# Optimization experiments

Measured on AMD Instinct MI355X. Metric: run time of the kernel, lower is better.

## Reference

```python
import jax, jax.numpy as jnp
import numpy as np

N, E, F, H, G = 50000, 640000, 128, 128, 64


def setup_inputs() -> dict:
    key = jax.random.key(0)
    ks = jax.random.split(key, 10)
    x = jax.random.normal(ks[0], (N, F), dtype=jnp.float32)
    edge_index = jax.random.randint(ks[1], (2, E), 0, N)
    batch = jnp.sort(jax.random.randint(ks[2], (N,), 0, G))

    def glorot(k, shp):
        return jax.random.normal(k, shp, dtype=jnp.float32) * np.float32(1.0 / np.sqrt(shp[0]))

    W1 = glorot(ks[3], (F, H)); b1 = jnp.zeros((H,), jnp.float32)
    W2 = glorot(ks[4], (H, H)); b2 = jnp.zeros((H,), jnp.float32)
    W3 = glorot(ks[5], (H, H)); b3 = jnp.zeros((H,), jnp.float32)
    W4 = glorot(ks[6], (H, 2)); b4 = jnp.zeros((2,), jnp.float32)
    return {"x": x, "W1": W1, "b1": b1, "W2": W2, "b2": b2,
            "W3": W3, "b3": b3, "W4": W4, "b4": b4,
            "edge_index": edge_index, "batch": batch, "num_graphs": G}


def reference(x, W1, b1, W2, b2, W3, b3, W4, b4, edge_index, batch, num_graphs):
    n = x.shape[0]
    loop = jnp.arange(n, dtype=edge_index.dtype)
    src = jnp.concatenate([edge_index[0], loop])  # with self-loops (PyG GCNConv default)
    dst = jnp.concatenate([edge_index[1], loop])
    # symmetric degree normalization: D^{-1/2} (A+I) D^{-1/2}
    deg = jax.ops.segment_sum(jnp.ones_like(src, dtype=x.dtype), dst, num_segments=n)
    dinv = jnp.where(deg > 0, jax.lax.rsqrt(deg), 0.0)
    norm = (dinv[src] * dinv[dst])[:, None]  # [E+N, 1]

    def gcn_conv(h, W, b):
        m = h @ W                                   # transform first (F->H), then propagate
        agg = jax.ops.segment_sum(m[src] * norm, dst, num_segments=n)
        return agg + b

    h = jax.nn.relu(gcn_conv(x, W1, b1))
    h = jax.nn.relu(gcn_conv(h, W2, b2))
    g = jax.ops.segment_max(h, batch, num_segments=num_graphs)  # global_max_pool
    z = jax.nn.relu(g @ W3 + b3)                    # dropout is identity in eval
    logits = z @ W4 + b4
    return jax.nn.log_softmax(logits, axis=1)
```

## Files before the change

### kernel.cpp

```cpp
#include <hip/hip_runtime.h>
#include <hip/hip_bf16.h>
#include <math.h>

#define HDIM 128
#define SCAN_B 256
#define NBLK 256

typedef short bfrag __attribute__((ext_vector_type(8)));
typedef float f32x4 __attribute__((ext_vector_type(4)));

__device__ inline unsigned short f2bf_rne(float x) {
    unsigned u = __float_as_uint(x);
    u = (u + 0x7fffu + ((u >> 16) & 1u)) >> 16;
    return (unsigned short)u;
}
__device__ inline float bf_lo(unsigned u) { return __uint_as_float(u << 16); }
__device__ inline float bf_hi(unsigned u) { return __uint_as_float(u & 0xffff0000u); }


__device__ inline void hist_body(int b, const int* __restrict__ dst,
                                 int* __restrict__ hist, int E, int chunk) {
    int start = b * chunk, end = min(E, start + chunk);
    for (int e = start + threadIdx.x; e < end; e += 256)
        atomicAdd(&hist[dst[e]], 1);
}

__device__ inline void wfrag_body(int b, const float* __restrict__ W1,
                                  const float* __restrict__ W2,
                                  unsigned short* __restrict__ w1h,
                                  unsigned short* __restrict__ w1l,
                                  unsigned short* __restrict__ w2h,
                                  unsigned short* __restrict__ w2l) {
    const float* W = (b < 64) ? W1 : W2;
    unsigned short* whi = (b < 64) ? w1h : w2h;
    unsigned short* wlo = (b < 64) ? w1l : w2l;
    int idx = (b & 63) * 256 + threadIdx.x;
    int k = idx >> 7;
    int n = idx & 127;
    int kt = k >> 5, q = (k >> 3) & 3, j = k & 7;
    int lm = n >> 3, nt = n & 7;
    int lane = q * 16 + lm;
    int o = ((kt * 8 + nt) * 64 + lane) * 8 + j;
    float x = W[idx];
    unsigned short hb = f2bf_rne(x);
    float hf = __uint_as_float(((unsigned)hb) << 16);
    unsigned short lb = f2bf_rne(x - hf);
    whi[o] = hb;
    wlo[o] = lb;
}

__device__ inline void scatter_body(int b, const int* __restrict__ srcv,
                                    const int* __restrict__ dstv,
                                    int* __restrict__ cursor,
                                    int* __restrict__ csr,
                                    int E, int chunk) {
    int start = b * chunk, end = min(E, start + chunk);
    for (int e = start + threadIdx.x; e < end; e += 256) {
        int pos = atomicAdd(&cursor[dstv[e]], 1);
        csr[pos] = srcv[e];
    }
}

#define GBM 64
__device__ inline void gemm_f32_body(int b, const float* __restrict__ A,
                                     const unsigned short* __restrict__ whi,
                                     const unsigned short* __restrict__ wlo,
                                     const float* __restrict__ dinv,
                                     unsigned short* __restrict__ C, int Nrows) {
    int tid = threadIdx.x;
    int w = tid >> 6, L = tid & 63;
    int lm = L & 15, lq = L >> 4;
    int row0 = b * GBM + w * 16;

    f32x4 acc[8];
#pragma unroll
    for (int nt = 0; nt < 8; ++nt) acc[nt] = (f32x4)(0.f);

#pragma unroll
    for (int kt = 0; kt < 4; ++kt) {
        int gr = row0 + lm;
        float4 v0 = make_float4(0.f, 0.f, 0.f, 0.f);
        float4 v1 = v0;
        if (gr < Nrows) {
            const float* p = &A[(size_t)gr * HDIM + kt * 32 + lq * 8];
            v0 = *(const float4*)p;
            v1 = *(const float4*)(p + 4);
        }
        float xv[8] = {v0.x, v0.y, v0.z, v0.w, v1.x, v1.y, v1.z, v1.w};
        bfrag ah, al;
#pragma unroll
        for (int j = 0; j < 8; ++j) {
            float x = xv[j];
            unsigned short hb = f2bf_rne(x);
            float hf = __uint_as_float(((unsigned)hb) << 16);
            unsigned short lb = f2bf_rne(x - hf);
            ah[j] = (short)hb;
            al[j] = (short)lb;
        }
#pragma unroll
        for (int nt = 0; nt < 8; ++nt) {
            int o = ((kt * 8 + nt) * 64 + L) * 8;
            bfrag wh = *(const bfrag*)&whi[o];
            bfrag wl = *(const bfrag*)&wlo[o];
            acc[nt] = __builtin_amdgcn_mfma_f32_16x16x32_bf16(ah, wh, acc[nt], 0, 0, 0);
            acc[nt] = __builtin_amdgcn_mfma_f32_16x16x32_bf16(al, wh, acc[nt], 0, 0, 0);
            acc[nt] = __builtin_amdgcn_mfma_f32_16x16x32_bf16(ah, wl, acc[nt], 0, 0, 0);
        }
    }

#pragma unroll
    for (int i = 0; i < 4; ++i) {
        int gr = row0 + lq * 4 + i;
        if (gr < Nrows) {
            float dd = dinv[gr];
            bfrag e;
#pragma unroll
            for (int nt = 0; nt < 8; ++nt) e[nt] = (short)f2bf_rne(dd * acc[nt][i]);
            *(bfrag*)&C[(size_t)gr * HDIM + lm * 8] = e;
        }
    }
}

__global__ __launch_bounds__(256) void mega1_kernel(const int* __restrict__ dst,
                                                    int* __restrict__ hist, int E,
                                                    int chunk,
                                                    const float* __restrict__ W1,
                                                    const float* __restrict__ W2,
                                                    unsigned short* __restrict__ w1h,
                                                    unsigned short* __restrict__ w1l,
                                                    unsigned short* __restrict__ w2h,
                                                    unsigned short* __restrict__ w2l) {
    int b = blockIdx.x;
    if (b < NBLK) hist_body(b, dst, hist, E, chunk);
    else wfrag_body(b - NBLK, W1, W2, w1h, w1l, w2h, w2l);
}

__global__ __launch_bounds__(256) void mega3_kernel(const int* __restrict__ srcv,
                                                    const int* __restrict__ dstv,
                                                    int* __restrict__ cursor,
                                                    int* __restrict__ csr,
                                                    int E, int chunk,
                                                    const float* __restrict__ A,
                                                    const unsigned short* __restrict__ whi,
                                                    const unsigned short* __restrict__ wlo,
                                                    const float* __restrict__ dinv,
                                                    unsigned short* __restrict__ C, int Nrows) {
    int b = blockIdx.x;
    if (b < NBLK) scatter_body(b, srcv, dstv, cursor, csr, E, chunk);
    else gemm_f32_body(b - NBLK, A, whi, wlo, dinv, C, Nrows);
}

__global__ __launch_bounds__(SCAN_B) void scan1_kernel(const int* __restrict__ in,
                                                       int* __restrict__ out,
                                                       int* __restrict__ sums, int n) {
    __shared__ int s[SCAN_B];
    int t = threadIdx.x;
    int idx = blockIdx.x * SCAN_B + t;
    int v = (idx < n) ? in[idx] : 0;
    s[t] = v;
    __syncthreads();
    for (int off = 1; off < SCAN_B; off <<= 1) {
        int x = (t >= off) ? s[t - off] : 0;
        __syncthreads();
        s[t] += x;
        __syncthreads();
    }
    if (idx < n) out[idx] = s[t];
    if (t == SCAN_B - 1) sums[blockIdx.x] = s[t];
}

__global__ __launch_bounds__(SCAN_B) void scan3_kernel(const int* __restrict__ in,
                                                       const int* __restrict__ incl,
                                                       const int* __restrict__ sums,
                                                       int* __restrict__ rowstart,
                                                       int* __restrict__ cursor,
                                                       float* __restrict__ dinv,
                                                       int n, int E) {
    __shared__ int s[SCAN_B];
    int t = threadIdx.x;
    int b = blockIdx.x;
    s[t] = (t < b) ? sums[t] : 0;
    __syncthreads();
    for (int off = SCAN_B / 2; off > 0; off >>= 1) {
        if (t < off) s[t] += s[t + off];
        __syncthreads();
    }
    int base = s[0];
    int idx = b * SCAN_B + t;
    if (idx < n) {
        int d = in[idx];
        int excl = incl[idx] - d + base;
        rowstart[idx] = excl;
        cursor[idx] = excl;
        dinv[idx] = rsqrtf((float)(d + 1));
        if (idx == n - 1) rowstart[idx + 1] = E;
    }
}

#define QACC(UV)                                       \
    acc[0] += bf_lo((UV).x); acc[1] += bf_hi((UV).x);  \
    acc[2] += bf_lo((UV).y); acc[3] += bf_hi((UV).y);  \
    acc[4] += bf_lo((UV).z); acc[5] += bf_hi((UV).z);  \
    acc[6] += bf_lo((UV).w); acc[7] += bf_hi((UV).w);

__device__ inline void qgather(const uint4* __restrict__ m4,
                               const int* __restrict__ csr,
                               int p, int pend, int t, float* acc) {
    for (; p + 8 <= pend; p += 8) {
        int s0 = csr[p], s1 = csr[p + 1], s2 = csr[p + 2], s3 = csr[p + 3];
        int s4 = csr[p + 4], s5 = csr[p + 5], s6 = csr[p + 6], s7 = csr[p + 7];
        uint4 u0 = m4[(size_t)s0 * 16 + t];
        uint4 u1 = m4[(size_t)s1 * 16 + t];
        uint4 u2 = m4[(size_t)s2 * 16 + t];
        uint4 u3 = m4[(size_t)s3 * 16 + t];
        uint4 u4 = m4[(size_t)s4 * 16 + t];
        uint4 u5 = m4[(size_t)s5 * 16 + t];
        uint4 u6 = m4[(size_t)s6 * 16 + t];
        uint4 u7 = m4[(size_t)s7 * 16 + t];
        QACC(u0); QACC(u1); QACC(u2); QACC(u3);
        QACC(u4); QACC(u5); QACC(u6); QACC(u7);
    }
    if (p + 4 <= pend) {
        int s0 = csr[p], s1 = csr[p + 1], s2 = csr[p + 2], s3 = csr[p + 3];
        uint4 u0 = m4[(size_t)s0 * 16 + t];
        uint4 u1 = m4[(size_t)s1 * 16 + t];
        uint4 u2 = m4[(size_t)s2 * 16 + t];
        uint4 u3 = m4[(size_t)s3 * 16 + t];
        QACC(u0); QACC(u1); QACC(u2); QACC(u3);
        p += 4;
    }
    if (p + 2 <= pend) {
        int s0 = csr[p], s1 = csr[p + 1];
        uint4 u0 = m4[(size_t)s0 * 16 + t];
        uint4 u1 = m4[(size_t)s1 * 16 + t];
        QACC(u0); QACC(u1);
        p += 2;
    }
    if (p < pend) {
        int s0 = csr[p];
        uint4 u0 = m4[(size_t)s0 * 16 + t];
        QACC(u0);
    }
}

__global__ __launch_bounds__(256) void agg_gemm_kernel(
        const uint4* __restrict__ m4,
        const int* __restrict__ rowstart,
        const int* __restrict__ csr,
        const float* __restrict__ dinv,
        const float* __restrict__ bias,
        const unsigned short* __restrict__ whi,
        const unsigned short* __restrict__ wlo,
        uint4* __restrict__ out_m, int n) {
    __shared__ unsigned short hbuf[16][HDIM + 8];
    __shared__ float cbuf[16][HDIM + 4];
    int t = threadIdx.x & 15;
    int nl = threadIdx.x >> 4;
    int node = blockIdx.x * 16 + nl;

    float dd = 0.f;
    unsigned short hv[8] = {0, 0, 0, 0, 0, 0, 0, 0};
    if (node < n) {
        dd = dinv[node];
        float acc[8];
        uint4 u = m4[(size_t)node * 16 + t];
        acc[0] = bf_lo(u.x); acc[1] = bf_hi(u.x);
        acc[2] = bf_lo(u.y); acc[3] = bf_hi(u.y);
        acc[4] = bf_lo(u.z); acc[5] = bf_hi(u.z);
        acc[6] = bf_lo(u.w); acc[7] = bf_hi(u.w);
        qgather(m4, csr, rowstart[node], rowstart[node + 1], t, acc);
        float4 b0 = *(const float4*)&bias[t * 8];
        float4 b1 = *(const float4*)&bias[t * 8 + 4];
        float bb[8] = {b0.x, b0.y, b0.z, b0.w, b1.x, b1.y, b1.z, b1.w};
#pragma unroll
        for (int j = 0; j < 8; ++j)
            hv[j] = f2bf_rne(fmaxf(fmaf(dd, acc[j], bb[j]), 0.f));
    }
    *(uint4*)&hbuf[nl][t * 8] = *(uint4*)hv;
    __syncthreads();

    int w = threadIdx.x >> 6, L = threadIdx.x & 63;
    int lm = L & 15, lq = L >> 4;
    f32x4 acc2[2];
    acc2[0] = (f32x4)(0.f);
    acc2[1] = (f32x4)(0.f);
#pragma unroll
    for (int kt = 0; kt < 4; ++kt) {
        bfrag a = *(const bfrag*)&hbuf[lm][kt * 32 + lq * 8];
#pragma unroll
        for (int q2 = 0; q2 < 2; ++q2) {
            int nt = w * 2 + q2;
            int o = ((kt * 8 + nt) * 64 + L) * 8;
            bfrag wh = *(const bfrag*)&whi[o];
            bfrag wl = *(const bfrag*)&wlo[o];
            acc2[q2] = __builtin_amdgcn_mfma_f32_16x16x32_bf16(a, wh, acc2[q2], 0, 0, 0);
            acc2[q2] = __builtin_amdgcn_mfma_f32_16x16x32_bf16(a, wl, acc2[q2], 0, 0, 0);
        }
    }
#pragma unroll
    for (int q2 = 0; q2 < 2; ++q2) {
        int nt = w * 2 + q2;
#pragma unroll
        for (int i = 0; i < 4; ++i) cbuf[lq * 4 + i][lm * 8 + nt] = acc2[q2][i];
    }
    __syncthreads();

    if (node < n) {
        float4 r0 = *(const float4*)&cbuf[nl][t * 8];
        float4 r1 = *(const float4*)&cbuf[nl][t * 8 + 4];
        unsigned short ev[8];
        ev[0] = f2bf_rne(dd * r0.x); ev[1] = f2bf_rne(dd * r0.y);
        ev[2] = f2bf_rne(dd * r0.z); ev[3] = f2bf_rne(dd * r0.w);
        ev[4] = f2bf_rne(dd * r1.x); ev[5] = f2bf_rne(dd * r1.y);
        ev[6] = f2bf_rne(dd * r1.z); ev[7] = f2bf_rne(dd * r1.w);
        out_m[(size_t)node * 16 + t] = *(uint4*)ev;
    }
}

__global__ __launch_bounds__(256) void agg_pool_kernel(const uint4* __restrict__ m4,
                                                       const int* __restrict__ rowstart,
                                                       const int* __restrict__ csr,
                                                       const float* __restrict__ dinv,
                                                       const float* __restrict__ bias,
                                                       const int* __restrict__ batch,
                                                       unsigned int* __restrict__ g, int n) {
    __shared__ float smx[16][HDIM];
    __shared__ int sgid[16];
    int t = threadIdx.x & 15;
    int nl = threadIdx.x >> 4;
    int node = blockIdx.x * 16 + nl;
    bool valid = node < n;
    if (valid) {
        float dd = dinv[node];
        float acc[8];
        uint4 u = m4[(size_t)node * 16 + t];
        acc[0] = bf_lo(u.x); acc[1] = bf_hi(u.x);
        acc[2] = bf_lo(u.y); acc[3] = bf_hi(u.y);
        acc[4] = bf_lo(u.z); acc[5] = bf_hi(u.z);
        acc[6] = bf_lo(u.w); acc[7] = bf_hi(u.w);
        qgather(m4, csr, rowstart[node], rowstart[node + 1], t, acc);
        float4 b0 = *(const float4*)&bias[t * 8];
        float4 b1 = *(const float4*)&bias[t * 8 + 4];
        float4 r0, r1;
        r0.x = fmaxf(fmaf(dd, acc[0], b0.x), 0.f);
        r0.y = fmaxf(fmaf(dd, acc[1], b0.y), 0.f);
        r0.z = fmaxf(fmaf(dd, acc[2], b0.z), 0.f);
        r0.w = fmaxf(fmaf(dd, acc[3], b0.w), 0.f);
        r1.x = fmaxf(fmaf(dd, acc[4], b1.x), 0.f);
        r1.y = fmaxf(fmaf(dd, acc[5], b1.y), 0.f);
        r1.z = fmaxf(fmaf(dd, acc[6], b1.z), 0.f);
        r1.w = fmaxf(fmaf(dd, acc[7], b1.w), 0.f);
        *(float4*)&smx[nl][t * 8] = r0;
        *(float4*)&smx[nl][t * 8 + 4] = r1;
    }
    if (t == 0) sgid[nl] = valid ? batch[node] : -1;
    __syncthreads();
    if (threadIdx.x < HDIM) {
        int c = threadIdx.x;
        int curg = -1;
        float run = 0.f;
#pragma unroll
        for (int r = 0; r < 16; ++r) {
            int gg = sgid[r];
            if (gg < 0) continue;
            if (gg != curg) {
                if (curg >= 0) atomicMax(&g[curg * HDIM + c], __float_as_uint(run));
                curg = gg;
                run = smx[r][c];
            } else {
                run = fmaxf(run, smx[r][c]);
            }
        }
        if (curg >= 0) atomicMax(&g[curg * HDIM + c], __float_as_uint(run));
    }
}

__global__ __launch_bounds__(128) void mlp_kernel(const unsigned int* __restrict__ gbits,
                                                  const float* __restrict__ W3,
                                                  const float* __restrict__ b3,
                                                  const float* __restrict__ W4,
                                                  const float* __restrict__ b4,
                                                  float* __restrict__ out) {
    __shared__ float gs[HDIM];
    __shared__ float r0[HDIM];
    __shared__ float r1[HDIM];
    int j = threadIdx.x;
    int b = blockIdx.x;
    gs[j] = __uint_as_float(gbits[b * HDIM + j]);
    __syncthreads();
    float acc = b3[j];
#pragma unroll 8
    for (int k = 0; k < HDIM; ++k) acc = fmaf(gs[k], W3[k * HDIM + j], acc);
    float z = fmaxf(acc, 0.f);
    r0[j] = z * W4[j * 2 + 0];
    r1[j] = z * W4[j * 2 + 1];
    __syncthreads();
    for (int off = 64; off > 0; off >>= 1) {
        if (j < off) {
            r0[j] += r0[j + off];
            r1[j] += r1[j + off];
        }
        __syncthreads();
    }
    if (j == 0) {
        float l0 = r0[0] + b4[0];
        float l1 = r1[0] + b4[1];
        float mx = fmaxf(l0, l1);
        float lse = mx + logf(expf(l0 - mx) + expf(l1 - mx));
        out[b * 2 + 0] = l0 - lse;
        out[b * 2 + 1] = l1 - lse;
    }
}

extern "C" void kernel_launch(void* const* d_in, const int* in_sizes, int n_in,
                              void* d_out, int out_size, void* d_ws, size_t ws_size,
                              hipStream_t stream) {
    const float* x  = (const float*)d_in[0];
    const float* W1 = (const float*)d_in[1];
    const float* b1 = (const float*)d_in[2];
    const float* W2 = (const float*)d_in[3];
    const float* b2 = (const float*)d_in[4];
    const float* W3 = (const float*)d_in[5];
    const float* b3 = (const float*)d_in[6];
    const float* W4 = (const float*)d_in[7];
    const float* b4 = (const float*)d_in[8];
    const int* ei    = (const int*)d_in[9];
    const int* batch = (const int*)d_in[10];

    const int N = in_sizes[0] / HDIM;
    const int E = in_sizes[9] / 2;
    const int G = out_size / 2;
    const int* src = ei;
    const int* dst = ei + E;

    const int chunk = (E + NBLK - 1) / NBLK;

    const int Nr = ((N + 63) / 64) * 64;
    char* wsb = (char*)d_ws;
    size_t o = 0;
    unsigned int* g = (unsigned int*)(wsb + o); o += (size_t)G * HDIM * 4;
    int* hist = (int*)(wsb + o);           o += (size_t)Nr * 4;
    size_t zero_bytes = o;
    int* hscan = (int*)(wsb + o);          o += (size_t)Nr * 4;
    int* sums = (int*)(wsb + o);           o += 256 * 4;
    int* rowstart = (int*)(wsb + o);       o += (size_t)(Nr + 64) * 4;
    int* cursor = (int*)(wsb + o);         o += (size_t)Nr * 4;
    float* dinv = (float*)(wsb + o);       o += (size_t)Nr * 4;
    int* csr = (int*)(wsb + o);            o += (size_t)E * 4;
    unsigned short* wf1h = (unsigned short*)(wsb + o); o += (size_t)HDIM * HDIM * 2;
    unsigned short* wf1l = (unsigned short*)(wsb + o); o += (size_t)HDIM * HDIM * 2;
    unsigned short* wf2h = (unsigned short*)(wsb + o); o += (size_t)HDIM * HDIM * 2;
    unsigned short* wf2l = (unsigned short*)(wsb + o); o += (size_t)HDIM * HDIM * 2;
    unsigned short* m = (unsigned short*)(wsb + o);    o += (size_t)Nr * HDIM * 2;
    unsigned short* m2 = (unsigned short*)(wsb + o);   o += (size_t)Nr * HDIM * 2;
    (void)ws_size; (void)n_in;

    (void)hipMemsetAsync(d_ws, 0, zero_bytes, stream);

    int sblocks = (N + SCAN_B - 1) / SCAN_B;
    int gemm_blocks = (N + GBM - 1) / GBM;
    int agg_blocks = (N + 15) / 16;

    mega1_kernel<<<NBLK + 128, 256, 0, stream>>>(dst, hist, E, chunk,
                                                 W1, W2, wf1h, wf1l, wf2h, wf2l);
    scan1_kernel<<<sblocks, SCAN_B, 0, stream>>>(hist, hscan, sums, N);
    scan3_kernel<<<sblocks, SCAN_B, 0, stream>>>(hist, hscan, sums,
                                                 rowstart, cursor, dinv, N, E);
    mega3_kernel<<<NBLK + gemm_blocks, 256, 0, stream>>>(src, dst, cursor, csr,
                                                         E, chunk,
                                                         x, wf1h, wf1l, dinv, m, N);
    agg_gemm_kernel<<<agg_blocks, 256, 0, stream>>>((const uint4*)m, rowstart, csr,
                                                    dinv, b1, wf2h, wf2l,
                                                    (uint4*)m2, N);
    agg_pool_kernel<<<agg_blocks, 256, 0, stream>>>((const uint4*)m2, rowstart, csr,
                                                    dinv, b2, batch, g, N);
    mlp_kernel<<<G, 128, 0, stream>>>(g, W3, b3, W4, b4, (float*)d_out);
}
```

Baseline: 228.9 us.

## Build CSR via two-level bucketed counting sort with LDS atomics

Replaces the per-node global-atomic histogram and scatter with a two-pass bucketed sort. Edges are first bucketed by dst>>8 using LDS atomics and per-block bucket offsets, then a new per-bucket kernel sorts within each bucket into the final CSR. The aim is to cut contended global atomics and random scattered writes. In exchange it adds an extra kernel launch and an 8-byte-per-edge intermediate buffer. Per-node degrees are still counted with global atomics so dinv can be computed.

```diff
diff --git a/kernel.cpp b/kernel.cpp
--- a/kernel.cpp
+++ b/kernel.cpp
@@ -19,10 +19,20 @@
 
 
 __device__ inline void hist_body(int b, const int* __restrict__ dst,
-                                 int* __restrict__ hist, int E, int chunk) {
+                                 int* __restrict__ hist, int* __restrict__ deg,
+                                 int E, int chunk, int nbuck) {
+    __shared__ int hl[256];
+    int t = threadIdx.x;
+    hl[t] = 0;
+    __syncthreads();
     int start = b * chunk, end = min(E, start + chunk);
-    for (int e = start + threadIdx.x; e < end; e += 256)
-        atomicAdd(&hist[dst[e]], 1);
+    for (int e = start + t; e < end; e += 256) {
+        int d = dst[e];
+        atomicAdd(&hl[d >> 8], 1);
+        atomicAdd(&deg[d], 1);
+    }
+    __syncthreads();
+    if (t < nbuck) hist[t * NBLK + b] = hl[t];
 }
 
 __device__ inline void wfrag_body(int b, const float* __restrict__ W1,
@@ -51,13 +61,18 @@
 
 __device__ inline void scatter_body(int b, const int* __restrict__ srcv,
                                     const int* __restrict__ dstv,
-                                    int* __restrict__ cursor,
-                                    int* __restrict__ csr,
-                                    int E, int chunk) {
+                                    const int* __restrict__ hscan,
+                                    int2* __restrict__ sorted,
+                                    int E, int chunk, int nbuck) {
+    __shared__ int cur[256];
+    int t = threadIdx.x;
+    if (t < nbuck) cur[t] = hscan[t * NBLK + b];
+    __syncthreads();
     int start = b * chunk, end = min(E, start + chunk);
-    for (int e = start + threadIdx.x; e < end; e += 256) {
-        int pos = atomicAdd(&cursor[dstv[e]], 1);
-        csr[pos] = srcv[e];
+    for (int e = start + t; e < end; e += 256) {
+        int d = dstv[e];
+        int pos = atomicAdd(&cur[d >> 8], 1);
+        sorted[pos] = make_int2(srcv[e], d);
     }
 }
 
@@ -122,8 +137,9 @@
 }
 
 __global__ __launch_bounds__(256) void mega1_kernel(const int* __restrict__ dst,
-                                                    int* __restrict__ hist, int E,
-                                                    int chunk,
+                                                    int* __restrict__ hist,
+                                                    int* __restrict__ deg, int E,
+                                                    int chunk, int nbuck,
                                                     const float* __restrict__ W1,
                                                     const float* __restrict__ W2,
                                                     unsigned short* __restrict__ w1h,
@@ -131,28 +147,31 @@
                                                     unsigned short* __restrict__ w2h,
                                                     unsigned short* __restrict__ w2l) {
     int b = blockIdx.x;
-    if (b < NBLK) hist_body(b, dst, hist, E, chunk);
+    if (b < NBLK) hist_body(b, dst, hist, deg, E, chunk, nbuck);
     else wfrag_body(b - NBLK, W1, W2, w1h, w1l, w2h, w2l);
 }
 
 __global__ __launch_bounds__(256) void mega3_kernel(const int* __restrict__ srcv,
                                                     const int* __restrict__ dstv,
-                                                    int* __restrict__ cursor,
-                                                    int* __restrict__ csr,
-                                                    int E, int chunk,
+                                                    const int* __restrict__ hscan,
+                                                    int2* __restrict__ sorted,
+                                                    int E, int chunk, int nbuck,
                                                     const float* __restrict__ A,
                                                     const unsigned short* __restrict__ whi,
                                                     const unsigned short* __restrict__ wlo,
                                                     const float* __restrict__ dinv,
                                                     unsigned short* __restrict__ C, int Nrows) {
     int b = blockIdx.x;
-    if (b < NBLK) scatter_body(b, srcv, dstv, cursor, csr, E, chunk);
+    if (b < NBLK) scatter_body(b, srcv, dstv, hscan, sorted, E, chunk, nbuck);
     else gemm_f32_body(b - NBLK, A, whi, wlo, dinv, C, Nrows);
 }
 
 __global__ __launch_bounds__(SCAN_B) void scan1_kernel(const int* __restrict__ in,
                                                        int* __restrict__ out,
-                                                       int* __restrict__ sums, int n) {
+                                                       int* __restrict__ sums,
+                                                       const int* __restrict__ deg,
+                                                       float* __restrict__ dinv,
+                                                       int n, int N) {
     __shared__ int s[SCAN_B];
     int t = threadIdx.x;
     int idx = blockIdx.x * SCAN_B + t;
@@ -167,15 +186,13 @@
     }
     if (idx < n) out[idx] = s[t];
     if (t == SCAN_B - 1) sums[blockIdx.x] = s[t];
+    if (idx < N) dinv[idx] = rsqrtf((float)(deg[idx] + 1));
 }
 
 __global__ __launch_bounds__(SCAN_B) void scan3_kernel(const int* __restrict__ in,
-                                                       const int* __restrict__ incl,
+                                                       int* __restrict__ inout,
                                                        const int* __restrict__ sums,
-                                                       int* __restrict__ rowstart,
-                                                       int* __restrict__ cursor,
-                                                       float* __restrict__ dinv,
-                                                       int n, int E) {
+                                                       int n) {
     __shared__ int s[SCAN_B];
     int t = threadIdx.x;
     int b = blockIdx.x;
@@ -187,13 +204,45 @@
     }
     int base = s[0];
     int idx = b * SCAN_B + t;
-    if (idx < n) {
-        int d = in[idx];
-        int excl = incl[idx] - d + base;
-        rowstart[idx] = excl;
-        cursor[idx] = excl;
-        dinv[idx] = rsqrtf((float)(d + 1));
-        if (idx == n - 1) rowstart[idx + 1] = E;
+    if (idx < n) inout[idx] = inout[idx] - in[idx] + base;
+}
+
+__global__ __launch_bounds__(256) void csr_kernel(const int2* __restrict__ sorted,
+                                                  const int* __restrict__ hscan,
+                                                  int* __restrict__ rowstart,
+                                                  int* __restrict__ csr,
+                                                  int N, int E, int nbuck) {
+    __shared__ int cnt[256];
+    __shared__ int s[256];
+    __shared__ int cur[256];
+    int b = blockIdx.x;
+    int t = threadIdx.x;
+    int start = hscan[b * NBLK];
+    int end = (b + 1 < nbuck) ? hscan[(b + 1) * NBLK] : E;
+    cnt[t] = 0;
+    __syncthreads();
+    for (int e = start + t; e < end; e += 256)
+        atomicAdd(&cnt[sorted[e].y & 255], 1);
+    __syncthreads();
+    int v = cnt[t];
+    s[t] = v;
+    __syncthreads();
+    for (int off = 1; off < 256; off <<= 1) {
+        int x = (t >= off) ? s[t - off] : 0;
+        __syncthreads();
+        s[t] += x;
+        __syncthreads();
+    }
+    int excl = s[t] - v;
+    int node = b * 256 + t;
+    if (node < N) rowstart[node] = start + excl;
+    if (b == nbuck - 1 && t == 0) rowstart[N] = E;
+    cur[t] = start + excl;
+    __syncthreads();
+    for (int e = start + t; e < end; e += 256) {
+        int2 ed = sorted[e];
+        int pos = atomicAdd(&cur[ed.y & 255], 1);
+        csr[pos] = ed.x;
     }
 }
 
@@ -433,19 +482,22 @@
     const int* src = ei;
     const int* dst = ei + E;
 
+    const int nbuck = (N + 255) >> 8;
+    const int nscan = nbuck * NBLK;
     const int chunk = (E + NBLK - 1) / NBLK;
 
     const int Nr = ((N + 63) / 64) * 64;
     char* wsb = (char*)d_ws;
     size_t o = 0;
     unsigned int* g = (unsigned int*)(wsb + o); o += (size_t)G * HDIM * 4;
-    int* hist = (int*)(wsb + o);           o += (size_t)Nr * 4;
+    int* hist = (int*)(wsb + o);           o += (size_t)nscan * 4;
+    int* deg = (int*)(wsb + o);            o += (size_t)Nr * 4;
     size_t zero_bytes = o;
-    int* hscan = (int*)(wsb + o);          o += (size_t)Nr * 4;
+    int* hscan = (int*)(wsb + o);          o += (size_t)nscan * 4;
     int* sums = (int*)(wsb + o);           o += 256 * 4;
     int* rowstart = (int*)(wsb + o);       o += (size_t)(Nr + 64) * 4;
-    int* cursor = (int*)(wsb + o);         o += (size_t)Nr * 4;
     float* dinv = (float*)(wsb + o);       o += (size_t)Nr * 4;
+    int2* sorted = (int2*)(wsb + o);       o += (size_t)E * 8;
     int* csr = (int*)(wsb + o);            o += (size_t)E * 4;
     unsigned short* wf1h = (unsigned short*)(wsb + o); o += (size_t)HDIM * HDIM * 2;
     unsigned short* wf1l = (unsigned short*)(wsb + o); o += (size_t)HDIM * HDIM * 2;
@@ -457,18 +509,18 @@
 
     (void)hipMemsetAsync(d_ws, 0, zero_bytes, stream);
 
-    int sblocks = (N + SCAN_B - 1) / SCAN_B;
+    int sblocks = (nscan + SCAN_B - 1) / SCAN_B;
     int gemm_blocks = (N + GBM - 1) / GBM;
     int agg_blocks = (N + 15) / 16;
 
-    mega1_kernel<<<NBLK + 128, 256, 0, stream>>>(dst, hist, E, chunk,
+    mega1_kernel<<<NBLK + 128, 256, 0, stream>>>(dst, hist, deg, E, chunk, nbuck,
                                                  W1, W2, wf1h, wf1l, wf2h, wf2l);
-    scan1_kernel<<<sblocks, SCAN_B, 0, stream>>>(hist, hscan, sums, N);
-    scan3_kernel<<<sblocks, SCAN_B, 0, stream>>>(hist, hscan, sums,
-                                                 rowstart, cursor, dinv, N, E);
-    mega3_kernel<<<NBLK + gemm_blocks, 256, 0, stream>>>(src, dst, cursor, csr,
-                                                         E, chunk,
+    scan1_kernel<<<sblocks, SCAN_B, 0, stream>>>(hist, hscan, sums, deg, dinv, nscan, N);
+    scan3_kernel<<<sblocks, SCAN_B, 0, stream>>>(hist, hscan, sums, nscan);
+    mega3_kernel<<<NBLK + gemm_blocks, 256, 0, stream>>>(src, dst, hscan, sorted,
+                                                         E, chunk, nbuck,
                                                          x, wf1h, wf1l, dinv, m, N);
+    csr_kernel<<<nbuck, 256, 0, stream>>>(sorted, hscan, rowstart, csr, N, E, nbuck);
     agg_gemm_kernel<<<agg_blocks, 256, 0, stream>>>((const uint4*)m, rowstart, csr,
                                                     dinv, b1, wf2h, wf2l,
                                                     (uint4*)m2, N);
```

New measurement: 218.5 us. 1.05x faster.
